# Performance work log

Measured on AMD Instinct MI355X. Metric: run time of the kernel, lower is better.

Reference implementation:

```python
import jax, jax.numpy as jnp
import numpy as np

N = 12        # ALL_QUBITS
COM_Q = 9     # COM_QUBITS
IMG_Q = 11    # IMG_QUBITS
LAYERS = 2
SQRT2 = float(np.sqrt(2.0))
H_GATE = jnp.asarray([[1.0, 1.0], [1.0, -1.0]], dtype=jnp.complex64) / SQRT2


def _bitrev_perm(q):
    # column j of the wires-1..q subspace corresponds to param index bitrev(j)
    idx = np.arange(2 ** q)
    rev = np.zeros_like(idx)
    for bpos in range(q):
        rev |= ((idx >> bpos) & 1) << (q - 1 - bpos)
    return rev


def _apply_1q(state, U, w):
    # state: (B, 2^N) complex; apply 2x2 gate U on wire w (wire 0 = MSB)
    B = state.shape[0]
    s = state.reshape(B, 2 ** w, 2, -1)
    return jnp.einsum('ij,bpjq->bpiq', U, s).reshape(B, -1)


def _apply_cnot(state, c, t):
    B = state.shape[0]
    s = state.reshape((B,) + (2,) * N)
    s0 = jax.lax.slice_in_dim(s, 0, 1, axis=c + 1)
    s1 = jnp.flip(jax.lax.slice_in_dim(s, 1, 2, axis=c + 1), axis=t + 1)
    return jnp.concatenate([s0, s1], axis=c + 1).reshape(B, -1)


def _frqi(state, angles, q):
    # Hadamards on wires 1..q, then uniformly-controlled RY(angles) on wire 0
    for w in range(1, q + 1):
        state = _apply_1q(state, H_GATE, w)
    rev = _bitrev_perm(q)
    half = 0.5 * angles[:, rev]            # (B, 2^q), angle per control column
    c = jnp.cos(half)[:, :, None]
    s = jnp.sin(half)[:, :, None]
    B = state.shape[0]
    st = state.reshape(B, 2, 2 ** q, -1)   # (B, wire0, wires1..q, rest)
    new0 = c * st[:, 0] - s * st[:, 1]
    new1 = s * st[:, 0] + c * st[:, 1]
    return jnp.stack([new0, new1], axis=1).reshape(B, -1)


def _rot(phi, theta, omega):
    # PennyLane Rot = RZ(omega) RY(theta) RZ(phi)
    c = jnp.cos(theta / 2)
    s = jnp.sin(theta / 2)
    m00 = jnp.exp(-0.5j * (phi + omega)) * c
    m01 = -jnp.exp(0.5j * (phi - omega)) * s
    m10 = jnp.exp(-0.5j * (phi - omega)) * s
    m11 = jnp.exp(0.5j * (phi + omega)) * c
    return jnp.stack([jnp.stack([m00, m01]), jnp.stack([m10, m11])])


def _circuit(com_params, img_params, qp):
    B = com_params.shape[0]
    state = jnp.zeros((B, 2 ** N), jnp.complex64).at[:, 0].set(1.0)
    state = _frqi(state, com_params, COM_Q)
    for l in range(LAYERS):  # StronglyEntanglingLayers
        for w in range(N):
            state = _apply_1q(state, _rot(qp[l, w, 0], qp[l, w, 1], qp[l, w, 2]), w)
        r = l % (N - 1) + 1  # default ranges
        for w in range(N):
            state = _apply_cnot(state, w, (w + r) % N)
    state = _frqi(state, img_params, IMG_Q)
    p = (jnp.abs(state.reshape(B, 2, -1)) ** 2).sum(axis=2)  # (B, 2) wire-0 probs
    return p[:, 1] - p[:, 0]  # expval of Hamiltonian = -1 * Z(0)


def setup_inputs() -> dict:
    key = jax.random.key(0)
    k1, k2, k3 = jax.random.split(key, 3)
    B = 1024
    x = jax.random.uniform(k1, (B, 2, 32, 32), dtype=jnp.float32)
    W = jax.random.normal(k2, (512, 2048), dtype=jnp.float32) * 0.02
    b = jnp.zeros((512,), dtype=jnp.float32)
    quantum_params = jax.random.uniform(k3, (LAYERS, N, 3), dtype=jnp.float32) * float(np.pi)
    return {"x": x, "W": W, "b": b, "quantum_params": quantum_params}


def reference(x, W, b, quantum_params):
    B = x.shape[0]
    xf = x.reshape(B, -1)                 # (B, 2048) img_params
    com = xf @ W.T + b                    # (B, 512) classical_nn output
    return _circuit(com, xf, quantum_params)
```

## Files before the change

kernel.cpp:

```cpp
#include <hip/hip_runtime.h>
#include <hip/hip_bf16.h>
#include <math.h>

#define RS2f 0.70710678118654752f

typedef __attribute__((ext_vector_type(8))) short bf16x8;
typedef __attribute__((ext_vector_type(4))) float f32x4;

__device__ __forceinline__ float bf2f(unsigned short h) {
    return __uint_as_float(((unsigned)h) << 16);
}
__device__ __forceinline__ ushort2 pk2(float a, float b) {
    union { __hip_bfloat162 h; ushort2 s; } u;
    u.h = __float22bfloat162_rn(make_float2(a, b));
    return u.s;
}

__global__ __launch_bounds__(256) void gemm_fused(const float* __restrict__ A,
                                                  const float* __restrict__ B,
                                                  float* __restrict__ P, int nch) {
    __shared__ short As[64 * 136];
    __shared__ short Bs[64 * 136];
    const int tid = threadIdx.x, lane = tid & 63, wv = tid >> 6;
    const int quad = lane >> 4, mrow = lane & 15;
    const int m0 = blockIdx.x * 64, n0 = blockIdx.y * 64;
    const int kb = blockIdx.z * nch * 64;
    const int srow = tid >> 2;
    const int sc = (tid & 3) * 16;

    f32x4 acc[4];
    #pragma unroll
    for (int j = 0; j < 4; ++j) acc[j] = (f32x4){0.f, 0.f, 0.f, 0.f};

    const float* Arow = A + (size_t)(m0 + srow) * 2048 + kb + sc;
    const float* Brow = B + (size_t)(n0 + srow) * 2048 + kb + sc;

    float4 av[4], bv[4];
    #pragma unroll
    for (int i = 0; i < 4; ++i) { av[i] = *(const float4*)(Arow + 4*i);
                                  bv[i] = *(const float4*)(Brow + 4*i); }

    for (int ch = 0; ch < nch; ++ch) {
        __syncthreads();
        #pragma unroll
        for (int i = 0; i < 4; ++i) {
            ushort2 h0 = pk2(av[i].x, av[i].y);
            ushort2 h1 = pk2(av[i].z, av[i].w);
            ushort2 l0 = pk2(av[i].x - bf2f(h0.x), av[i].y - bf2f(h0.y));
            ushort2 l1 = pk2(av[i].z - bf2f(h1.x), av[i].w - bf2f(h1.y));
            *(ushort4*)&As[srow * 136 + sc + 4*i]      = make_ushort4(h0.x, h0.y, h1.x, h1.y);
            *(ushort4*)&As[srow * 136 + 64 + sc + 4*i] = make_ushort4(l0.x, l0.y, l1.x, l1.y);
            h0 = pk2(bv[i].x, bv[i].y);
            h1 = pk2(bv[i].z, bv[i].w);
            l0 = pk2(bv[i].x - bf2f(h0.x), bv[i].y - bf2f(h0.y));
            l1 = pk2(bv[i].z - bf2f(h1.x), bv[i].w - bf2f(h1.y));
            *(ushort4*)&Bs[srow * 136 + sc + 4*i]      = make_ushort4(h0.x, h0.y, h1.x, h1.y);
            *(ushort4*)&Bs[srow * 136 + 64 + sc + 4*i] = make_ushort4(l0.x, l0.y, l1.x, l1.y);
        }
        __syncthreads();
        if (ch + 1 < nch) {
            const int o = (ch + 1) * 64;
            #pragma unroll
            for (int i = 0; i < 4; ++i) { av[i] = *(const float4*)(Arow + o + 4*i);
                                          bv[i] = *(const float4*)(Brow + o + 4*i); }
        }
        #pragma unroll
        for (int s = 0; s < 4; ++s) {
            const int off = s * 32 + quad * 8;
            bf16x8 af = *(const bf16x8*)&As[(wv * 16 + mrow) * 136 + off];
            #pragma unroll
            for (int j = 0; j < 4; ++j) {
                bf16x8 bf = *(const bf16x8*)&Bs[(j * 16 + mrow) * 136 + off];
                acc[j] = __builtin_amdgcn_mfma_f32_16x16x32_bf16(af, bf, acc[j], 0, 0, 0);
            }
        }
    }
    float* Pz = P + (size_t)blockIdx.z * 524288;
    #pragma unroll
    for (int j = 0; j < 4; ++j)
        #pragma unroll
        for (int r = 0; r < 4; ++r)
            Pz[(m0 + wv * 16 + quad * 4 + r) * 512 + n0 + j * 16 + mrow] = acc[j][r];
}

__global__ __launch_bounds__(256) void reduce_kernel(float* __restrict__ P,
                                                     const float* __restrict__ bias,
                                                     int SK) {
    int i = blockIdx.x * 256 + threadIdx.x;
    float s = bias[i & 511];
    for (int z = 0; z < SK; ++z) s += P[(size_t)z * 524288 + i];
    P[i] = s;
}

__global__ __launch_bounds__(256) void gemm_f32(const float* __restrict__ A,
                                                const float* __restrict__ W,
                                                float* __restrict__ C) {
    __shared__ float Asf[64][33];
    __shared__ float Bsf[32][33];
    const int tid = threadIdx.x;
    const int m0 = blockIdx.x * 64;
    const int n0 = blockIdx.y * 32;
    const int tm = tid >> 4, tn = tid & 15;
    float acc[4][2] = {};
    for (int k0 = 0; k0 < 2048; k0 += 32) {
        #pragma unroll
        for (int i = 0; i < 8; ++i) {
            int idx = tid + i * 256;
            Asf[idx >> 5][idx & 31] = A[(m0 + (idx >> 5)) * 2048 + k0 + (idx & 31)];
        }
        #pragma unroll
        for (int i = 0; i < 4; ++i) {
            int idx = tid + i * 256;
            Bsf[idx >> 5][idx & 31] = W[(n0 + (idx >> 5)) * 2048 + k0 + (idx & 31)];
        }
        __syncthreads();
        #pragma unroll
        for (int kk = 0; kk < 32; ++kk) {
            float a0 = Asf[tm*4+0][kk], a1 = Asf[tm*4+1][kk];
            float a2 = Asf[tm*4+2][kk], a3 = Asf[tm*4+3][kk];
            float b0 = Bsf[tn*2+0][kk], b1 = Bsf[tn*2+1][kk];
            acc[0][0] += a0*b0; acc[0][1] += a0*b1;
            acc[1][0] += a1*b0; acc[1][1] += a1*b1;
            acc[2][0] += a2*b0; acc[2][1] += a2*b1;
            acc[3][0] += a3*b0; acc[3][1] += a3*b1;
        }
        __syncthreads();
    }
    #pragma unroll
    for (int r = 0; r < 4; ++r)
        #pragma unroll
        for (int c = 0; c < 2; ++c)
            C[(m0 + tm*4 + r) * 512 + n0 + tn*2 + c] = acc[r][c];
}

struct CMat { float m00r,m00i,m01r,m01i,m10r,m10i,m11r,m11i; };

__device__ __forceinline__ CMat mk_rot(const float* __restrict__ qp, int l, int w) {
    const float* g = qp + (l * 12 + w) * 3;
    float phi = g[0], th = g[1], om = g[2];
    float st, ct, sa, ca, sb, cb;
    sincosf(0.5f * th, &st, &ct);
    sincosf(0.5f * (phi + om), &sa, &ca);
    sincosf(0.5f * (phi - om), &sb, &cb);
    CMat M;
    M.m00r =  ct * ca; M.m00i = -ct * sa;
    M.m01r = -st * cb; M.m01i = -st * sb;
    M.m10r =  st * cb; M.m10i = -st * sb;
    M.m11r =  ct * ca; M.m11i =  ct * sa;
    return M;
}

template<int W> struct WI {
    static constexpr int kind = (W == 0 || W == 7) ? 2 : ((W >= 1 && W <= 6) ? 1 : 0);
    static constexpr int eb   = (W >= 8) ? (11 - W) : 0;
    static constexpr int lm   = (W >= 1 && W <= 6) ? (1 << (6 - W)) : 0;
    static constexpr int vm   = (W == 0) ? 2 : ((W == 7) ? 1 : 0);
};

__device__ __forceinline__ void exch_put(float* xbuf, int slot,
                                         const float vr[16], const float vi[16]) {
    __syncthreads();
    float4* p = (float4*)xbuf;
    #pragma unroll
    for (int j = 0; j < 8; ++j)
        p[(j << 8) + slot] = make_float4(vr[2*j], vi[2*j], vr[2*j+1], vi[2*j+1]);
    __syncthreads();
}

__device__ __forceinline__ void shfl_perm(float vr[16], float vi[16], int src) {
    #pragma unroll
    for (int e = 0; e < 16; ++e) {
        vr[e] = __shfl(vr[e], src, 64);
        vi[e] = __shfl(vi[e], src, 64);
    }
}

template<int EB>
__device__ __forceinline__ void rot_local(float vr[16], float vi[16], const CMat& M) {
    #pragma unroll
    for (int e = 0; e < 16; ++e) if (!(e & (1 << EB))) {
        const int e1 = e | (1 << EB);
        float x0r = vr[e],  x0i = vi[e];
        float x1r = vr[e1], x1i = vi[e1];
        vr[e]  = M.m00r*x0r - M.m00i*x0i + M.m01r*x1r - M.m01i*x1i;
        vi[e]  = M.m00r*x0i + M.m00i*x0r + M.m01r*x1i + M.m01i*x1r;
        vr[e1] = M.m10r*x0r - M.m10i*x0i + M.m11r*x1r - M.m11i*x1i;
        vi[e1] = M.m10r*x0i + M.m10i*x0r + M.m11r*x1i + M.m11i*x1r;
    }
}

template<int LM>
__device__ __forceinline__ void rot_lane(float vr[16], float vi[16], int lane, const CMat& M) {
    const bool hi = lane & LM;
    const float Ar = hi ? M.m11r : M.m00r, Ai = hi ? M.m11i : M.m00i;
    const float Br = hi ? M.m10r : M.m01r, Bi = hi ? M.m10i : M.m01i;
    #pragma unroll
    for (int e = 0; e < 16; ++e) {
        float pr = __shfl_xor(vr[e], LM, 64);
        float pi = __shfl_xor(vi[e], LM, 64);
        float orr = vr[e], oi = vi[e];
        vr[e] = Ar*orr - Ai*oi + Br*pr - Bi*pi;
        vi[e] = Ar*oi + Ai*orr + Br*pi + Bi*pr;
    }
}

template<int VM>
__device__ __forceinline__ void rot_wave(float vr[16], float vi[16], float* xbuf,
                                         int waveId, int lane, const CMat& M) {
    exch_put(xbuf, (waveId << 6) + lane, vr, vi);
    const float4* p = (const float4*)xbuf;
    const int ps = ((waveId ^ VM) << 6) + lane;
    const bool hi = waveId & VM;
    const float Ar = hi ? M.m11r : M.m00r, Ai = hi ? M.m11i : M.m00i;
    const float Br = hi ? M.m10r : M.m01r, Bi = hi ? M.m10i : M.m01i;
    #pragma unroll
    for (int j = 0; j < 8; ++j) {
        float4 q = p[(j << 8) + ps];
        const int e0 = 2*j, e1 = 2*j + 1;
        float r0 = vr[e0], i0 = vi[e0], r1 = vr[e1], i1 = vi[e1];
        vr[e0] = Ar*r0 - Ai*i0 + Br*q.x - Bi*q.y;
        vi[e0] = Ar*i0 + Ai*r0 + Br*q.y + Bi*q.x;
        vr[e1] = Ar*r1 - Ai*i1 + Br*q.z - Bi*q.w;
        vi[e1] = Ar*i1 + Ai*r1 + Br*q.w + Bi*q.z;
    }
}

template<int W>
__device__ __forceinline__ void rot_wire(float vr[16], float vi[16], float* xbuf,
                                         int waveId, int lane, const CMat& M) {
    if constexpr (WI<W>::kind == 0)      rot_local<WI<W>::eb>(vr, vi, M);
    else if constexpr (WI<W>::kind == 1) rot_lane<WI<W>::lm>(vr, vi, lane, M);
    else                                 rot_wave<WI<W>::vm>(vr, vi, xbuf, waveId, lane, M);
}

template<int C, int T>
__device__ __forceinline__ void cnot(float vr[16], float vi[16], float* xbuf,
                                     int waveId, int lane) {
    constexpr int ck = WI<C>::kind, tk = WI<T>::kind;
    if constexpr (ck == 0 && tk == 0) {
        constexpr int cb = 1 << WI<C>::eb, tb = 1 << WI<T>::eb;
        #pragma unroll
        for (int e = 0; e < 16; ++e) if ((e & cb) && !(e & tb)) {
            const int e1 = e | tb;
            float t = vr[e]; vr[e] = vr[e1]; vr[e1] = t;
            t = vi[e]; vi[e] = vi[e1]; vi[e1] = t;
        }
    } else if constexpr (ck == 0 && tk == 1) {
        constexpr int cb = 1 << WI<C>::eb, tm = WI<T>::lm;
        #pragma unroll
        for (int e = 0; e < 16; ++e) if (e & cb) {
            vr[e] = __shfl_xor(vr[e], tm, 64);
            vi[e] = __shfl_xor(vi[e], tm, 64);
        }
    } else if constexpr (ck == 0 && tk == 2) {
        constexpr int cb = 1 << WI<C>::eb, vm = WI<T>::vm;
        exch_put(xbuf, (waveId << 6) + lane, vr, vi);
        const float4* p = (const float4*)xbuf;
        const int ps = ((waveId ^ vm) << 6) + lane;
        #pragma unroll
        for (int j = 0; j < 8; ++j) {
            if ((((2*j) & cb) != 0) || (((2*j+1) & cb) != 0)) {
                float4 q = p[(j << 8) + ps];
                if (((2*j) & cb) != 0)   { vr[2*j]   = q.x; vi[2*j]   = q.y; }
                if (((2*j+1) & cb) != 0) { vr[2*j+1] = q.z; vi[2*j+1] = q.w; }
            }
        }
    } else if constexpr (ck == 1 && tk == 0) {
        constexpr int cm = WI<C>::lm, tb = 1 << WI<T>::eb;
        const bool cc = lane & cm;
        #pragma unroll
        for (int e = 0; e < 16; ++e) if (!(e & tb)) {
            const int e1 = e | tb;
            float a = vr[e], bb = vr[e1];
            vr[e] = cc ? bb : a; vr[e1] = cc ? a : bb;
            a = vi[e]; bb = vi[e1];
            vi[e] = cc ? bb : a; vi[e1] = cc ? a : bb;
        }
    } else if constexpr (ck == 1 && tk == 1) {
        constexpr int cm = WI<C>::lm, tm = WI<T>::lm;
        const int src = (lane & cm) ? (lane ^ tm) : lane;
        shfl_perm(vr, vi, src);
    } else if constexpr (ck == 1 && tk == 2) {
        constexpr int cm = WI<C>::lm, vm = WI<T>::vm;
        exch_put(xbuf, (waveId << 6) + lane, vr, vi);
        const float4* p = (const float4*)xbuf;
        const int ps = ((waveId ^ vm) << 6) + lane;
        const bool take = lane & cm;
        #pragma unroll
        for (int j = 0; j < 8; ++j) {
            float4 q = p[(j << 8) + ps];
            vr[2*j]   = take ? q.x : vr[2*j];   vi[2*j]   = take ? q.y : vi[2*j];
            vr[2*j+1] = take ? q.z : vr[2*j+1]; vi[2*j+1] = take ? q.w : vi[2*j+1];
        }
    } else if constexpr (ck == 2 && tk == 0) {
        constexpr int vm = WI<C>::vm, tb = 1 << WI<T>::eb;
        if (waveId & vm) {
            #pragma unroll
            for (int e = 0; e < 16; ++e) if (!(e & tb)) {
                const int e1 = e | tb;
                float t = vr[e]; vr[e] = vr[e1]; vr[e1] = t;
                t = vi[e]; vi[e] = vi[e1]; vi[e1] = t;
            }
        }
    } else {
        constexpr int vm = WI<C>::vm, tm = WI<T>::lm;
        if (waveId & vm) {
            #pragma unroll
            for (int e = 0; e < 16; ++e) {
                vr[e] = __shfl_xor(vr[e], tm, 64);
                vi[e] = __shfl_xor(vi[e], tm, 64);
            }
        }
    }
}

template<int W>
__device__ __forceinline__ void h_wire(float vr[16], float vi[16], float* xbuf,
                                       int waveId, int lane) {
    if constexpr (WI<W>::kind == 0) {
        constexpr int tb = 1 << WI<W>::eb;
        #pragma unroll
        for (int e = 0; e < 16; ++e) if (!(e & tb)) {
            const int e1 = e | tb;
            float x0 = vr[e], x1 = vr[e1];
            vr[e] = (x0 + x1) * RS2f; vr[e1] = (x0 - x1) * RS2f;
            x0 = vi[e]; x1 = vi[e1];
            vi[e] = (x0 + x1) * RS2f; vi[e1] = (x0 - x1) * RS2f;
        }
    } else if constexpr (WI<W>::kind == 1) {
        constexpr int m = WI<W>::lm;
        const float sgn = (lane & m) ? -RS2f : RS2f;
        #pragma unroll
        for (int e = 0; e < 16; ++e) {
            float pr = __shfl_xor(vr[e], m, 64);
            float pi = __shfl_xor(vi[e], m, 64);
            vr[e] = pr * RS2f + vr[e] * sgn;
            vi[e] = pi * RS2f + vi[e] * sgn;
        }
    } else {
        constexpr int vm = WI<W>::vm;
        exch_put(xbuf, (waveId << 6) + lane, vr, vi);
        const float4* p = (const float4*)xbuf;
        const int ps = ((waveId ^ vm) << 6) + lane;
        const float sgn = (waveId & vm) ? -RS2f : RS2f;
        #pragma unroll
        for (int j = 0; j < 8; ++j) {
            float4 q = p[(j << 8) + ps];
            vr[2*j]   = q.x * RS2f + vr[2*j]   * sgn;
            vi[2*j]   = q.y * RS2f + vi[2*j]   * sgn;
            vr[2*j+1] = q.z * RS2f + vr[2*j+1] * sgn;
            vi[2*j+1] = q.w * RS2f + vi[2*j+1] * sgn;
        }
    }
}

__global__ __launch_bounds__(256) void circuit_sa(const float* __restrict__ com,
                                                  const float* __restrict__ xf,
                                                  const float* __restrict__ qp,
                                                  float* __restrict__ out) {
    __shared__ float xbuf[8192];
    __shared__ float ang[2048];
    const int tid = threadIdx.x, lane = tid & 63, waveId = tid >> 6;
    const int b = blockIdx.x;
    if (tid < 128) ((float4*)ang)[tid] = ((const float4*)(com + b * 512))[tid];
    __syncthreads();
    float vr[16], vi[16];
    #pragma unroll
    for (int e = 0; e < 16; ++e) { vr[e] = 0.0f; vi[e] = 0.0f; }
    const float K9 = 0.044194173824159216f;
    #pragma unroll
    for (int m = 0; m < 4; ++m) {
        int j = (lane << 3) | ((waveId & 1) << 2) | m;
        int rj = (int)(__brev((unsigned)j) >> 23);
        float s, c;
        sincosf(0.5f * ang[rj], &s, &c);
        vr[m << 2] = K9 * ((waveId & 2) ? s : c);
    }
    #pragma unroll 1
    for (int l = 0; l < 2; ++l) {
        { CMat M = mk_rot(qp, l, 0);  rot_wire<0 >(vr, vi, xbuf, waveId, lane, M); }
        { CMat M = mk_rot(qp, l, 1);  rot_wire<1 >(vr, vi, xbuf, waveId, lane, M); }
        { CMat M = mk_rot(qp, l, 2);  rot_wire<2 >(vr, vi, xbuf, waveId, lane, M); }
        { CMat M = mk_rot(qp, l, 3);  rot_wire<3 >(vr, vi, xbuf, waveId, lane, M); }
        { CMat M = mk_rot(qp, l, 4);  rot_wire<4 >(vr, vi, xbuf, waveId, lane, M); }
        { CMat M = mk_rot(qp, l, 5);  rot_wire<5 >(vr, vi, xbuf, waveId, lane, M); }
        { CMat M = mk_rot(qp, l, 6);  rot_wire<6 >(vr, vi, xbuf, waveId, lane, M); }
        { CMat M = mk_rot(qp, l, 7);  rot_wire<7 >(vr, vi, xbuf, waveId, lane, M); }
        { CMat M = mk_rot(qp, l, 8);  rot_wire<8 >(vr, vi, xbuf, waveId, lane, M); }
        { CMat M = mk_rot(qp, l, 9);  rot_wire<9 >(vr, vi, xbuf, waveId, lane, M); }
        { CMat M = mk_rot(qp, l, 10); rot_wire<10>(vr, vi, xbuf, waveId, lane, M); }
        { CMat M = mk_rot(qp, l, 11); rot_wire<11>(vr, vi, xbuf, waveId, lane, M); }
        if (l == 0) {
            int j = lane;
            j ^= (j & 2)  ? 1  : 0;
            j ^= (j & 4)  ? 2  : 0;
            j ^= (j & 8)  ? 4  : 0;
            j ^= (j & 16) ? 8  : 0;
            j ^= (j & 32) ? 16 : 0;
            j ^= (waveId & 2) ? 32 : 0;
            shfl_perm(vr, vi, j);
            cnot<6,7>(vr,vi,xbuf,waveId,lane);   cnot<7,8>(vr,vi,xbuf,waveId,lane);
            cnot<8,9>(vr,vi,xbuf,waveId,lane);   cnot<9,10>(vr,vi,xbuf,waveId,lane);
            cnot<10,11>(vr,vi,xbuf,waveId,lane); cnot<11,0>(vr,vi,xbuf,waveId,lane);
        } else {
            int j = lane;
            j ^= (j & 4)  ? 1  : 0;
            j ^= (j & 8)  ? 2  : 0;
            j ^= (j & 16) ? 4  : 0;
            j ^= (j & 32) ? 8  : 0;
            j ^= (waveId & 2) ? 16 : 0;
            shfl_perm(vr, vi, j);
            cnot<5,7>(vr,vi,xbuf,waveId,lane);   cnot<6,8>(vr,vi,xbuf,waveId,lane);
            cnot<7,9>(vr,vi,xbuf,waveId,lane);   cnot<8,10>(vr,vi,xbuf,waveId,lane);
            cnot<9,11>(vr,vi,xbuf,waveId,lane);  cnot<10,0>(vr,vi,xbuf,waveId,lane);
            cnot<11,1>(vr,vi,xbuf,waveId,lane);
        }
    }
    h_wire<1>(vr,vi,xbuf,waveId,lane);  h_wire<2>(vr,vi,xbuf,waveId,lane);
    h_wire<3>(vr,vi,xbuf,waveId,lane);  h_wire<4>(vr,vi,xbuf,waveId,lane);
    h_wire<5>(vr,vi,xbuf,waveId,lane);  h_wire<6>(vr,vi,xbuf,waveId,lane);
    h_wire<7>(vr,vi,xbuf,waveId,lane);  h_wire<8>(vr,vi,xbuf,waveId,lane);
    h_wire<9>(vr,vi,xbuf,waveId,lane);  h_wire<10>(vr,vi,xbuf,waveId,lane);
    h_wire<11>(vr,vi,xbuf,waveId,lane);
    {
        const float4* x4 = (const float4*)(xf + b * 2048);
        ((float4*)ang)[tid]       = x4[tid];
        ((float4*)ang)[tid + 256] = x4[tid + 256];
    }
    __syncthreads();
    exch_put(xbuf, (waveId << 6) + lane, vr, vi);
    {
        const float4* p = (const float4*)xbuf;
        const int ps = ((waveId ^ 2) << 6) + lane;
        const bool hi = waveId & 2;
        float acc = 0.0f;
        #pragma unroll
        for (int j = 0; j < 8; ++j) {
            float4 q = p[(j << 8) + ps];
            #pragma unroll
            for (int h = 0; h < 2; ++h) {
                const int e = 2*j + h;
                const float prr = h ? q.z : q.x;
                const float pii = h ? q.w : q.y;
                int v = (lane << 5) | ((waveId & 1) << 4) | e;
                int rv = (int)(__brev((unsigned)v) >> 21);
                float s, c;
                sincosf(0.5f * ang[rv], &s, &c);
                float nr = hi ? (s*prr + c*vr[e]) : (c*vr[e] - s*prr);
                float ni = hi ? (s*pii + c*vi[e]) : (c*vi[e] - s*pii);
                acc += nr*nr + ni*ni;
            }
        }
        if (!hi) acc = -acc;
        #pragma unroll
        for (int off = 32; off > 0; off >>= 1) acc += __shfl_down(acc, off, 64);
        __syncthreads();
        if (lane == 0) xbuf[waveId] = acc;
        __syncthreads();
        if (tid == 0) out[b] = xbuf[0] + xbuf[1] + xbuf[2] + xbuf[3];
    }
}

extern "C" void kernel_launch(void* const* d_in, const int* in_sizes, int n_in,
                              void* d_out, int out_size, void* d_ws, size_t ws_size,
                              hipStream_t stream) {
    const float* x    = (const float*)d_in[0];
    const float* W    = (const float*)d_in[1];
    const float* bias = (const float*)d_in[2];
    const float* qp   = (const float*)d_in[3];
    float* out = (float*)d_out;

    const size_t SLAB = 2097152;
    float* P = (float*)d_ws;
    if (ws_size >= 2 * SLAB) {
        int SK = 2;
        if      (ws_size >= 8 * SLAB) SK = 8;
        else if (ws_size >= 4 * SLAB) SK = 4;
        dim3 g(16, 8, SK);
        gemm_fused<<<g, 256, 0, stream>>>(x, W, P, 32 / SK);
        reduce_kernel<<<2048, 256, 0, stream>>>(P, bias, SK);
        circuit_sa<<<1024, 256, 0, stream>>>(P, x, qp, out);
    } else {
        dim3 g(16, 16);
        gemm_f32<<<g, 256, 0, stream>>>(x, W, P);
        reduce_kernel<<<2048, 256, 0, stream>>>(P, bias, 1);
        circuit_sa<<<1024, 256, 0, stream>>>(P, x, qp, out);
    }
}
```

Measured before the change: 149.7 us.

## Remap GEMM blocks per XCD, cache rotation matrices in LDS, use fast sincos

The split-K GEMM grid is flattened to 1D and each block index is remapped so that the blocks landing on one XCD (bid & 7) share a 4x4 patch of M/N tiles, improving L2 reuse of A and W rows. In the circuit kernel the 24 Rot matrices are built once per block into shared memory instead of being recomputed inside the layer loop. The FRQI sincosf calls are replaced with the __sinf/__cosf intrinsics, which cost less but are less accurate at large angles.

```diff
diff --git a/kernel.cpp b/kernel.cpp
--- a/kernel.cpp
+++ b/kernel.cpp
@@ -23,8 +23,14 @@
     __shared__ short Bs[64 * 136];
     const int tid = threadIdx.x, lane = tid & 63, wv = tid >> 6;
     const int quad = lane >> 4, mrow = lane & 15;
-    const int m0 = blockIdx.x * 64, n0 = blockIdx.y * 64;
-    const int kb = blockIdx.z * nch * 64;
+    const int bid = blockIdx.x;
+    const int xcd = bid & 7;
+    const int idx = bid >> 3;
+    const int mt  = ((xcd >> 1) << 2) | (idx & 3);
+    const int nt  = ((xcd & 1) << 2) | ((idx >> 2) & 3);
+    const int zt  = idx >> 4;
+    const int m0 = mt * 64, n0 = nt * 64;
+    const int kb = zt * nch * 64;
     const int srow = tid >> 2;
     const int sc = (tid & 3) * 16;
 
@@ -75,7 +81,7 @@
             }
         }
     }
-    float* Pz = P + (size_t)blockIdx.z * 524288;
+    float* Pz = P + (size_t)zt * 524288;
     #pragma unroll
     for (int j = 0; j < 4; ++j)
         #pragma unroll
@@ -360,9 +366,14 @@
                                                   float* __restrict__ out) {
     __shared__ float xbuf[8192];
     __shared__ float ang[2048];
+    __shared__ CMat cms[24];
     const int tid = threadIdx.x, lane = tid & 63, waveId = tid >> 6;
     const int b = blockIdx.x;
     if (tid < 128) ((float4*)ang)[tid] = ((const float4*)(com + b * 512))[tid];
+    if (tid >= 128 && tid < 152) {
+        const int t = tid - 128;
+        cms[t] = mk_rot(qp, t / 12, t % 12);
+    }
     __syncthreads();
     float vr[16], vi[16];
     #pragma unroll
@@ -372,24 +383,25 @@
     for (int m = 0; m < 4; ++m) {
         int j = (lane << 3) | ((waveId & 1) << 2) | m;
         int rj = (int)(__brev((unsigned)j) >> 23);
-        float s, c;
-        sincosf(0.5f * ang[rj], &s, &c);
+        float h = 0.5f * ang[rj];
+        float s = __sinf(h), c = __cosf(h);
         vr[m << 2] = K9 * ((waveId & 2) ? s : c);
     }
     #pragma unroll 1
     for (int l = 0; l < 2; ++l) {
-        { CMat M = mk_rot(qp, l, 0);  rot_wire<0 >(vr, vi, xbuf, waveId, lane, M); }
-        { CMat M = mk_rot(qp, l, 1);  rot_wire<1 >(vr, vi, xbuf, waveId, lane, M); }
-        { CMat M = mk_rot(qp, l, 2);  rot_wire<2 >(vr, vi, xbuf, waveId, lane, M); }
-        { CMat M = mk_rot(qp, l, 3);  rot_wire<3 >(vr, vi, xbuf, waveId, lane, M); }
-        { CMat M = mk_rot(qp, l, 4);  rot_wire<4 >(vr, vi, xbuf, waveId, lane, M); }
-        { CMat M = mk_rot(qp, l, 5);  rot_wire<5 >(vr, vi, xbuf, waveId, lane, M); }
-        { CMat M = mk_rot(qp, l, 6);  rot_wire<6 >(vr, vi, xbuf, waveId, lane, M); }
-        { CMat M = mk_rot(qp, l, 7);  rot_wire<7 >(vr, vi, xbuf, waveId, lane, M); }
-        { CMat M = mk_rot(qp, l, 8);  rot_wire<8 >(vr, vi, xbuf, waveId, lane, M); }
-        { CMat M = mk_rot(qp, l, 9);  rot_wire<9 >(vr, vi, xbuf, waveId, lane, M); }
-        { CMat M = mk_rot(qp, l, 10); rot_wire<10>(vr, vi, xbuf, waveId, lane, M); }
-        { CMat M = mk_rot(qp, l, 11); rot_wire<11>(vr, vi, xbuf, waveId, lane, M); }
+        const CMat* cl = &cms[l * 12];
+        rot_wire<0 >(vr, vi, xbuf, waveId, lane, cl[0]);
+        rot_wire<1 >(vr, vi, xbuf, waveId, lane, cl[1]);
+        rot_wire<2 >(vr, vi, xbuf, waveId, lane, cl[2]);
+        rot_wire<3 >(vr, vi, xbuf, waveId, lane, cl[3]);
+        rot_wire<4 >(vr, vi, xbuf, waveId, lane, cl[4]);
+        rot_wire<5 >(vr, vi, xbuf, waveId, lane, cl[5]);
+        rot_wire<6 >(vr, vi, xbuf, waveId, lane, cl[6]);
+        rot_wire<7 >(vr, vi, xbuf, waveId, lane, cl[7]);
+        rot_wire<8 >(vr, vi, xbuf, waveId, lane, cl[8]);
+        rot_wire<9 >(vr, vi, xbuf, waveId, lane, cl[9]);
+        rot_wire<10>(vr, vi, xbuf, waveId, lane, cl[10]);
+        rot_wire<11>(vr, vi, xbuf, waveId, lane, cl[11]);
         if (l == 0) {
             int j = lane;
             j ^= (j & 2)  ? 1  : 0;
@@ -444,8 +456,8 @@
                 const float pii = h ? q.w : q.y;
                 int v = (lane << 5) | ((waveId & 1) << 4) | e;
                 int rv = (int)(__brev((unsigned)v) >> 21);
-                float s, c;
-                sincosf(0.5f * ang[rv], &s, &c);
+                float ha = 0.5f * ang[rv];
+                float s = __sinf(ha), c = __cosf(ha);
                 float nr = hi ? (s*prr + c*vr[e]) : (c*vr[e] - s*prr);
                 float ni = hi ? (s*pii + c*vi[e]) : (c*vi[e] - s*pii);
                 acc += nr*nr + ni*ni;
@@ -476,8 +488,7 @@
         int SK = 2;
         if      (ws_size >= 8 * SLAB) SK = 8;
         else if (ws_size >= 4 * SLAB) SK = 4;
-        dim3 g(16, 8, SK);
-        gemm_fused<<<g, 256, 0, stream>>>(x, W, P, 32 / SK);
+        gemm_fused<<<dim3(128 * SK), 256, 0, stream>>>(x, W, P, 32 / SK);
         reduce_kernel<<<2048, 256, 0, stream>>>(P, bias, SK);
         circuit_sa<<<1024, 256, 0, stream>>>(P, x, qp, out);
     } else {
```

After: 144.3 us. 1.04x faster.
